# Kernel optimization log

Hardware: AMD Instinct MI355X
Metric: run time of the kernel (lower is better)

Reference implementation:

```python
import jax, jax.numpy as jnp
import numpy as np

B, S, H, NH = 8, 1024, 512, 8
HD = H // NH  # 64
ALPHA = 32.0


def setup_inputs() -> dict:
    key = jax.random.key(0)
    ks = jax.random.split(key, 8)
    hidden_states = jax.random.normal(ks[0], (B, S, H), dtype=jnp.float32)
    attention_mask = jnp.zeros((B, 1, 1, S), dtype=jnp.float32)
    rel_2d_pos = jax.random.normal(ks[1], (B, NH, S, S), dtype=jnp.float32)
    scale = 0.02
    Wq = jax.random.normal(ks[2], (H, H), dtype=jnp.float32) * scale
    Wk = jax.random.normal(ks[3], (H, H), dtype=jnp.float32) * scale
    Wv = jax.random.normal(ks[4], (H, H), dtype=jnp.float32) * scale
    bq = jnp.zeros((H,), dtype=jnp.float32)
    bk = jnp.zeros((H,), dtype=jnp.float32)
    bv = jnp.zeros((H,), dtype=jnp.float32)
    return {
        "hidden_states": hidden_states,
        "attention_mask": attention_mask,
        "rel_2d_pos": rel_2d_pos,
        "Wq": Wq, "bq": bq, "Wk": Wk, "bk": bk, "Wv": Wv, "bv": bv,
    }


def cogview_attention(scores, alpha=ALPHA):
    # scores / alpha -> amax -> softmax((s - max) * alpha); faithful to original
    scaled = scores / alpha
    max_value = jnp.max(scaled, axis=-1, keepdims=True)
    return jax.nn.softmax((scaled - max_value) * alpha, axis=-1)


def reference(hidden_states, attention_mask, rel_2d_pos, Wq, bq, Wk, bk, Wv, bv):
    b, s, _ = hidden_states.shape
    def split_heads(x):
        return x.reshape(b, s, NH, HD).transpose(0, 2, 1, 3)  # [B,NH,S,HD]
    q = split_heads(hidden_states @ Wq.T + bq)
    k = split_heads(hidden_states @ Wk.T + bk)
    v = split_heads(hidden_states @ Wv.T + bv)
    scale = 1.0 / jnp.sqrt(jnp.float32(HD))
    scores = jnp.einsum("bhqd,bhkd->bhqk", q * scale, k)
    scores = scores + rel_2d_pos  # spatial 2D relative bias
    scores = scores + attention_mask  # additive mask, broadcast [B,1,1,S]
    probs = cogview_attention(scores)
    ctx = jnp.einsum("bhqk,bhkd->bhqd", probs, v)
    ctx = ctx.transpose(0, 2, 1, 3).reshape(b, s, H)
    return ctx
```

## Files before the change

### kernel.cpp

```cpp
#include <hip/hip_runtime.h>

typedef _Float16 f16x8 __attribute__((ext_vector_type(8)));
typedef float    f32x4 __attribute__((ext_vector_type(4)));

#define MFMA16(a,b,c) __builtin_amdgcn_mfma_f32_16x16x32_f16((a),(b),(c),0,0,0)

constexpr int Bc  = 8;
constexpr int Sc  = 1024;
constexpr int Hc  = 512;
constexpr int NHc = 8;
constexpr int HDc = 64;

__global__ __launch_bounds__(256) void qkv_proj(
    const float* __restrict__ hs,
    const float* __restrict__ Wq, const float* __restrict__ bq,
    const float* __restrict__ Wk, const float* __restrict__ bk,
    const float* __restrict__ Wv, const float* __restrict__ bv,
    _Float16* __restrict__ qws, _Float16* __restrict__ kws,
    _Float16* __restrict__ vws)
{
    const int z  = blockIdx.z;
    const float* W   = (z == 0) ? Wq : (z == 1) ? Wk : Wv;
    const float* bia = (z == 0) ? bq : (z == 1) ? bk : bv;

    const int m0 = blockIdx.x * 64;
    const int n0 = blockIdx.y * 64;
    const int tid  = threadIdx.x;
    const int w    = tid >> 6;
    const int lane = tid & 63;
    const int l15  = lane & 15;
    const int quad = lane >> 4;

    __shared__ __align__(16) _Float16 As[64][40];
    __shared__ __align__(16) _Float16 Bs[64][40];

    f32x4 acc[4] = {};

    const int r = tid >> 2;
    const int c = (tid & 3) * 8;

    for (int kt = 0; kt < 16; ++kt) {
        const int k0 = kt * 32;
        const float4* ap = (const float4*)(hs + (size_t)(m0 + r) * 512 + k0 + c);
        const float4* bp = (const float4*)(W  + (size_t)(n0 + r) * 512 + k0 + c);
        float4 a0 = ap[0], a1 = ap[1];
        float4 b0 = bp[0], b1 = bp[1];
        __syncthreads();
        f16x8 av, bv8;
        av[0]=(_Float16)a0.x; av[1]=(_Float16)a0.y; av[2]=(_Float16)a0.z; av[3]=(_Float16)a0.w;
        av[4]=(_Float16)a1.x; av[5]=(_Float16)a1.y; av[6]=(_Float16)a1.z; av[7]=(_Float16)a1.w;
        bv8[0]=(_Float16)b0.x; bv8[1]=(_Float16)b0.y; bv8[2]=(_Float16)b0.z; bv8[3]=(_Float16)b0.w;
        bv8[4]=(_Float16)b1.x; bv8[5]=(_Float16)b1.y; bv8[6]=(_Float16)b1.z; bv8[7]=(_Float16)b1.w;
        *(f16x8*)&As[r][c] = av;
        *(f16x8*)&Bs[r][c] = bv8;
        __syncthreads();
        f16x8 af = *(const f16x8*)&As[w * 16 + l15][quad * 8];
#pragma unroll
        for (int nb = 0; nb < 4; ++nb) {
            f16x8 bf = *(const f16x8*)&Bs[nb * 16 + l15][quad * 8];
            acc[nb] = MFMA16(af, bf, acc[nb]);
        }
    }

#pragma unroll
    for (int nb = 0; nb < 4; ++nb) {
        const int n  = n0 + nb * 16 + l15;
        const float bvv = bia[n];
        const int h  = n >> 6;
        const int hd = n & 63;
#pragma unroll
        for (int rr = 0; rr < 4; ++rr) {
            const int m = m0 + w * 16 + quad * 4 + rr;
            const int b = m >> 10;
            const int s = m & 1023;
            const float val = acc[nb][rr] + bvv;
            if (z == 0)
                qws[(((size_t)(b * NHc + h)) * Sc + s) * HDc + hd] = (_Float16)val;
            else if (z == 1)
                kws[(((size_t)(b * NHc + h)) * Sc + s) * HDc + hd] = (_Float16)val;
            else
                vws[(((size_t)(b * NHc + h)) * HDc + hd) * Sc + s] = (_Float16)val;
        }
    }
}

__global__ __launch_bounds__(256) void attn(
    const _Float16* __restrict__ qws, const _Float16* __restrict__ kws,
    const _Float16* __restrict__ vws, const float* __restrict__ rel,
    const float* __restrict__ mask, float* __restrict__ out)
{
    const int qt = blockIdx.x;
    const int bh = blockIdx.y;
    const int b  = bh >> 3;
    const int h  = bh & 7;
    const int tid  = threadIdx.x;
    const int w    = tid >> 6;
    const int lane = tid & 63;
    const int l15  = lane & 15;
    const int quad = lane >> 4;
    const int q0w  = qt * 64 + w * 16;

    __shared__ __align__(16) _Float16 lds_p[4][16][72];

    const _Float16* qh = qws + (size_t)bh * Sc * HDc;
    const _Float16* kh = kws + (size_t)bh * Sc * HDc;
    const _Float16* vh = vws + (size_t)bh * HDc * Sc;
    const float* relh  = rel + (size_t)bh * Sc * Sc;
    const float* maskb = mask + (size_t)b * Sc;

    f16x8 qf0 = *(const f16x8*)(qh + (size_t)(q0w + l15) * HDc + quad * 8);
    f16x8 qf1 = *(const f16x8*)(qh + (size_t)(q0w + l15) * HDc + 32 + quad * 8);

    float m_run[4], l_run[4];
    f32x4 o[4] = {};
#pragma unroll
    for (int rj = 0; rj < 4; ++rj) { m_run[rj] = -1e30f; l_run[rj] = 0.f; }

    for (int kt = 0; kt < 16; ++kt) {
        const int kbase = kt * 64;

        f32x4 sc[4] = {};
#pragma unroll
        for (int nb = 0; nb < 4; ++nb) {
            const _Float16* kp = kh + (size_t)(kbase + nb * 16 + l15) * HDc + quad * 8;
            f16x8 kf0 = *(const f16x8*)kp;
            f16x8 kf1 = *(const f16x8*)(kp + 32);
            sc[nb] = MFMA16(qf0, kf0, sc[nb]);
            sc[nb] = MFMA16(qf1, kf1, sc[nb]);
        }

#pragma unroll
        for (int nb = 0; nb < 4; ++nb) {
            const int kcol = kbase + nb * 16 + l15;
            const float mk = maskb[kcol];
#pragma unroll
            for (int rj = 0; rj < 4; ++rj) {
                const int qrow = q0w + quad * 4 + rj;
                sc[nb][rj] = sc[nb][rj] * 0.125f + relh[(size_t)qrow * Sc + kcol] + mk;
            }
        }

#pragma unroll
        for (int rj = 0; rj < 4; ++rj) {
            float mx = fmaxf(fmaxf(sc[0][rj], sc[1][rj]), fmaxf(sc[2][rj], sc[3][rj]));
#pragma unroll
            for (int off = 1; off < 16; off <<= 1) mx = fmaxf(mx, __shfl_xor(mx, off));
            const float mnew  = fmaxf(m_run[rj], mx);
            const float alpha = __expf(m_run[rj] - mnew);
            float rs = 0.f;
#pragma unroll
            for (int nb = 0; nb < 4; ++nb) {
                const float p = __expf(sc[nb][rj] - mnew);
                sc[nb][rj] = p;
                rs += p;
            }
#pragma unroll
            for (int off = 1; off < 16; off <<= 1) rs += __shfl_xor(rs, off);
            m_run[rj] = mnew;
            l_run[rj] = l_run[rj] * alpha + rs;
            o[0][rj] *= alpha; o[1][rj] *= alpha; o[2][rj] *= alpha; o[3][rj] *= alpha;
        }

        __syncthreads();
#pragma unroll
        for (int nb = 0; nb < 4; ++nb)
#pragma unroll
            for (int rj = 0; rj < 4; ++rj)
                lds_p[w][quad * 4 + rj][nb * 16 + l15] = (_Float16)sc[nb][rj];
        __syncthreads();
        f16x8 ap0 = *(const f16x8*)&lds_p[w][l15][quad * 8];
        f16x8 ap1 = *(const f16x8*)&lds_p[w][l15][32 + quad * 8];

#pragma unroll
        for (int nb = 0; nb < 4; ++nb) {
            const _Float16* vp = vh + (size_t)(nb * 16 + l15) * Sc + kbase + quad * 8;
            f16x8 v0 = *(const f16x8*)vp;
            f16x8 v1 = *(const f16x8*)(vp + 32);
            o[nb] = MFMA16(ap0, v0, o[nb]);
            o[nb] = MFMA16(ap1, v1, o[nb]);
        }
    }

#pragma unroll
    for (int nb = 0; nb < 4; ++nb) {
#pragma unroll
        for (int rj = 0; rj < 4; ++rj) {
            const int qrow = q0w + quad * 4 + rj;
            out[((size_t)(b * Sc + qrow)) * Hc + h * HDc + nb * 16 + l15] =
                o[nb][rj] / l_run[rj];
        }
    }
}

extern "C" void kernel_launch(void* const* d_in, const int* in_sizes, int n_in,
                              void* d_out, int out_size, void* d_ws, size_t ws_size,
                              hipStream_t stream) {
    const float* hs   = (const float*)d_in[0];
    const float* mask = (const float*)d_in[1];
    const float* rel  = (const float*)d_in[2];
    const float* Wq   = (const float*)d_in[3];
    const float* bq   = (const float*)d_in[4];
    const float* Wk   = (const float*)d_in[5];
    const float* bk   = (const float*)d_in[6];
    const float* Wv   = (const float*)d_in[7];
    const float* bv   = (const float*)d_in[8];
    float* out = (float*)d_out;

    const size_t elems = (size_t)Bc * Sc * Hc;
    _Float16* qws = (_Float16*)d_ws;
    _Float16* kws = qws + elems;
    _Float16* vws = kws + elems;

    qkv_proj<<<dim3(128, 8, 3), 256, 0, stream>>>(hs, Wq, bq, Wk, bk, Wv, bv,
                                                  qws, kws, vws);
    attn<<<dim3(16, 64), 256, 0, stream>>>(qws, kws, vws, rel, mask, out);
}
```

Measured before the change: 510.5 us.

## Pre-convert inputs to fp16, use larger-tile QKV GEMM, prefetch rel bias

A separate kernel now converts hidden states and the three weight matrices to fp16. The QKV projection becomes one fused GEMM with 128x128 tiles and 16 accumulators per wave, loading tiles through global_load_lds. The attention kernel prefetches the next tile's rel_2d_pos values into registers, drops the block-wide barriers around the per-wave LDS probability tile, and multiplies by a reciprocal at the end. This trades an extra conversion pass and more registers for better GEMM reuse and latency hiding on the large fp32 bias stream. Removing the barriers relies on each wave using only its own LDS slice.

```diff
diff --git a/kernel.cpp b/kernel.cpp
--- a/kernel.cpp
+++ b/kernel.cpp
@@ -1,6 +1,7 @@
 #include <hip/hip_runtime.h>
 
 typedef _Float16 f16x8 __attribute__((ext_vector_type(8)));
+typedef _Float16 f16x4 __attribute__((ext_vector_type(4)));
 typedef float    f32x4 __attribute__((ext_vector_type(4)));
 
 #define MFMA16(a,b,c) __builtin_amdgcn_mfma_f32_16x16x32_f16((a),(b),(c),0,0,0)
@@ -11,75 +12,119 @@
 constexpr int NHc = 8;
 constexpr int HDc = 64;
 
-__global__ __launch_bounds__(256) void qkv_proj(
+__global__ __launch_bounds__(256) void cvt_f16(
     const float* __restrict__ hs,
-    const float* __restrict__ Wq, const float* __restrict__ bq,
-    const float* __restrict__ Wk, const float* __restrict__ bk,
-    const float* __restrict__ Wv, const float* __restrict__ bv,
+    const float* __restrict__ wq, const float* __restrict__ wk,
+    const float* __restrict__ wv,
+    _Float16* __restrict__ hs16, _Float16* __restrict__ w16)
+{
+    const size_t i4  = (size_t)blockIdx.x * 256 + threadIdx.x;
+    const size_t HS4 = (size_t)Bc * Sc * Hc / 4;
+    const size_t W4  = (size_t)Hc * Hc / 4;
+    float4 v;
+    _Float16* dst;
+    if (i4 < HS4) {
+        v = ((const float4*)hs)[i4];
+        dst = hs16 + i4 * 4;
+    } else {
+        const size_t j = i4 - HS4;
+        const int z = (int)(j / W4);
+        const size_t o = j - (size_t)z * W4;
+        const float* src = (z == 0) ? wq : (z == 1) ? wk : wv;
+        v = ((const float4*)src)[o];
+        dst = w16 + j * 4;
+    }
+    f16x4 h;
+    h[0] = (_Float16)v.x; h[1] = (_Float16)v.y;
+    h[2] = (_Float16)v.z; h[3] = (_Float16)v.w;
+    *(f16x4*)dst = h;
+}
+
+__global__ __launch_bounds__(256) void qkv_gemm(
+    const _Float16* __restrict__ A,
+    const _Float16* __restrict__ Bm,
+    const float* __restrict__ bq, const float* __restrict__ bk,
+    const float* __restrict__ bv,
     _Float16* __restrict__ qws, _Float16* __restrict__ kws,
     _Float16* __restrict__ vws)
 {
-    const int z  = blockIdx.z;
-    const float* W   = (z == 0) ? Wq : (z == 1) ? Wk : Wv;
-    const float* bia = (z == 0) ? bq : (z == 1) ? bk : bv;
-
-    const int m0 = blockIdx.x * 64;
-    const int n0 = blockIdx.y * 64;
+    __shared__ __align__(16) _Float16 As[128 * 64];
+    __shared__ __align__(16) _Float16 Bs[128 * 64];
+
+    const int m0 = blockIdx.x * 128;
+    const int n0 = blockIdx.y * 128;
     const int tid  = threadIdx.x;
+    const int lane = tid & 63;
     const int w    = tid >> 6;
-    const int lane = tid & 63;
     const int l15  = lane & 15;
     const int quad = lane >> 4;
-
-    __shared__ __align__(16) _Float16 As[64][40];
-    __shared__ __align__(16) _Float16 Bs[64][40];
-
-    f32x4 acc[4] = {};
-
-    const int r = tid >> 2;
-    const int c = (tid & 3) * 8;
-
-    for (int kt = 0; kt < 16; ++kt) {
-        const int k0 = kt * 32;
-        const float4* ap = (const float4*)(hs + (size_t)(m0 + r) * 512 + k0 + c);
-        const float4* bp = (const float4*)(W  + (size_t)(n0 + r) * 512 + k0 + c);
-        float4 a0 = ap[0], a1 = ap[1];
-        float4 b0 = bp[0], b1 = bp[1];
+    const int wm   = (w >> 1) * 64;
+    const int wn   = (w & 1) * 64;
+
+    f32x4 acc[4][4] = {};
+
+    const int srow = tid >> 3;
+    const int scol = (tid & 7) * 8;
+
+    for (int k0 = 0; k0 < 512; k0 += 64) {
         __syncthreads();
-        f16x8 av, bv8;
-        av[0]=(_Float16)a0.x; av[1]=(_Float16)a0.y; av[2]=(_Float16)a0.z; av[3]=(_Float16)a0.w;
-        av[4]=(_Float16)a1.x; av[5]=(_Float16)a1.y; av[6]=(_Float16)a1.z; av[7]=(_Float16)a1.w;
-        bv8[0]=(_Float16)b0.x; bv8[1]=(_Float16)b0.y; bv8[2]=(_Float16)b0.z; bv8[3]=(_Float16)b0.w;
-        bv8[4]=(_Float16)b1.x; bv8[5]=(_Float16)b1.y; bv8[6]=(_Float16)b1.z; bv8[7]=(_Float16)b1.w;
-        *(f16x8*)&As[r][c] = av;
-        *(f16x8*)&Bs[r][c] = bv8;
+#pragma unroll
+        for (int j = 0; j < 4; ++j) {
+            const _Float16* ga = A  + (size_t)(m0 + srow + 32 * j) * 512 + k0 + scol;
+            const _Float16* gb = Bm + (size_t)(n0 + srow + 32 * j) * 512 + k0 + scol;
+            __builtin_amdgcn_global_load_lds(
+                (const __attribute__((address_space(1))) void*)ga,
+                (__attribute__((address_space(3))) void*)(As + tid * 8 + j * 2048),
+                16, 0, 0);
+            __builtin_amdgcn_global_load_lds(
+                (const __attribute__((address_space(1))) void*)gb,
+                (__attribute__((address_space(3))) void*)(Bs + tid * 8 + j * 2048),
+                16, 0, 0);
+        }
         __syncthreads();
-        f16x8 af = *(const f16x8*)&As[w * 16 + l15][quad * 8];
-#pragma unroll
-        for (int nb = 0; nb < 4; ++nb) {
-            f16x8 bf = *(const f16x8*)&Bs[nb * 16 + l15][quad * 8];
-            acc[nb] = MFMA16(af, bf, acc[nb]);
-        }
-    }
-
+#pragma unroll
+        for (int ks = 0; ks < 2; ++ks) {
+            f16x8 af[4], bf[4];
+#pragma unroll
+            for (int i = 0; i < 4; ++i) {
+                af[i] = *(const f16x8*)&As[(wm + i * 16 + l15) * 64 + ks * 32 + quad * 8];
+                bf[i] = *(const f16x8*)&Bs[(wn + i * 16 + l15) * 64 + ks * 32 + quad * 8];
+            }
+#pragma unroll
+            for (int mb = 0; mb < 4; ++mb)
+#pragma unroll
+                for (int nb = 0; nb < 4; ++nb)
+                    acc[mb][nb] = MFMA16(af[mb], bf[nb], acc[mb][nb]);
+        }
+    }
+
+    const int zsel = n0 >> 9;
+    const float* bias = (zsel == 0) ? bq : (zsel == 1) ? bk : bv;
 #pragma unroll
     for (int nb = 0; nb < 4; ++nb) {
-        const int n  = n0 + nb * 16 + l15;
-        const float bvv = bia[n];
-        const int h  = n >> 6;
-        const int hd = n & 63;
-#pragma unroll
-        for (int rr = 0; rr < 4; ++rr) {
-            const int m = m0 + w * 16 + quad * 4 + rr;
+        const int n  = n0 + wn + nb * 16 + l15;
+        const int nn = n & 511;
+        const int h  = nn >> 6;
+        const int hd = nn & 63;
+        const float bvv = bias[nn];
+#pragma unroll
+        for (int mb = 0; mb < 4; ++mb) {
+            const int m = m0 + wm + mb * 16 + quad * 4;
             const int b = m >> 10;
             const int s = m & 1023;
-            const float val = acc[nb][rr] + bvv;
-            if (z == 0)
-                qws[(((size_t)(b * NHc + h)) * Sc + s) * HDc + hd] = (_Float16)val;
-            else if (z == 1)
-                kws[(((size_t)(b * NHc + h)) * Sc + s) * HDc + hd] = (_Float16)val;
-            else
-                vws[(((size_t)(b * NHc + h)) * HDc + hd) * Sc + s] = (_Float16)val;
+            if (zsel == 2) {
+                f16x4 t;
+#pragma unroll
+                for (int rr = 0; rr < 4; ++rr)
+                    t[rr] = (_Float16)(acc[mb][nb][rr] + bvv);
+                *(f16x4*)&vws[((size_t)(b * NHc + h) * HDc + hd) * Sc + s] = t;
+            } else {
+                _Float16* dst = (zsel == 0 ? qws : kws)
+                              + ((size_t)(b * NHc + h) * Sc + s) * HDc + hd;
+#pragma unroll
+                for (int rr = 0; rr < 4; ++rr)
+                    dst[(size_t)rr * HDc] = (_Float16)(acc[mb][nb][rr] + bvv);
+            }
         }
     }
 }
@@ -116,6 +161,15 @@
 #pragma unroll
     for (int rj = 0; rj < 4; ++rj) { m_run[rj] = -1e30f; l_run[rj] = 0.f; }
 
+    float rbuf[16];
+#pragma unroll
+    for (int nb = 0; nb < 4; ++nb)
+#pragma unroll
+        for (int rj = 0; rj < 4; ++rj)
+            rbuf[nb * 4 + rj] =
+                relh[(size_t)(q0w + quad * 4 + rj) * Sc + nb * 16 + l15];
+
+#pragma unroll
     for (int kt = 0; kt < 16; ++kt) {
         const int kbase = kt * 64;
 
@@ -129,15 +183,23 @@
             sc[nb] = MFMA16(qf1, kf1, sc[nb]);
         }
 
+        float rn[16];
+        if (kt < 15) {
+#pragma unroll
+            for (int nb = 0; nb < 4; ++nb)
+#pragma unroll
+                for (int rj = 0; rj < 4; ++rj)
+                    rn[nb * 4 + rj] =
+                        relh[(size_t)(q0w + quad * 4 + rj) * Sc
+                             + kbase + 64 + nb * 16 + l15];
+        }
+
 #pragma unroll
         for (int nb = 0; nb < 4; ++nb) {
-            const int kcol = kbase + nb * 16 + l15;
-            const float mk = maskb[kcol];
-#pragma unroll
-            for (int rj = 0; rj < 4; ++rj) {
-                const int qrow = q0w + quad * 4 + rj;
-                sc[nb][rj] = sc[nb][rj] * 0.125f + relh[(size_t)qrow * Sc + kcol] + mk;
-            }
+            const float mk = maskb[kbase + nb * 16 + l15];
+#pragma unroll
+            for (int rj = 0; rj < 4; ++rj)
+                sc[nb][rj] = sc[nb][rj] * 0.125f + rbuf[nb * 4 + rj] + mk;
         }
 
 #pragma unroll
@@ -161,13 +223,11 @@
             o[0][rj] *= alpha; o[1][rj] *= alpha; o[2][rj] *= alpha; o[3][rj] *= alpha;
         }
 
-        __syncthreads();
 #pragma unroll
         for (int nb = 0; nb < 4; ++nb)
 #pragma unroll
             for (int rj = 0; rj < 4; ++rj)
                 lds_p[w][quad * 4 + rj][nb * 16 + l15] = (_Float16)sc[nb][rj];
-        __syncthreads();
         f16x8 ap0 = *(const f16x8*)&lds_p[w][l15][quad * 8];
         f16x8 ap1 = *(const f16x8*)&lds_p[w][l15][32 + quad * 8];
 
@@ -179,16 +239,19 @@
             o[nb] = MFMA16(ap0, v0, o[nb]);
             o[nb] = MFMA16(ap1, v1, o[nb]);
         }
-    }
-
-#pragma unroll
-    for (int nb = 0; nb < 4; ++nb) {
-#pragma unroll
-        for (int rj = 0; rj < 4; ++rj) {
-            const int qrow = q0w + quad * 4 + rj;
+
+#pragma unroll
+        for (int i = 0; i < 16; ++i) rbuf[i] = rn[i];
+    }
+
+#pragma unroll
+    for (int rj = 0; rj < 4; ++rj) {
+        const float linv = 1.0f / l_run[rj];
+        const int qrow = q0w + quad * 4 + rj;
+#pragma unroll
+        for (int nb = 0; nb < 4; ++nb)
             out[((size_t)(b * Sc + qrow)) * Hc + h * HDc + nb * 16 + l15] =
-                o[nb][rj] / l_run[rj];
-        }
+                o[nb][rj] * linv;
     }
 }
 
@@ -207,11 +270,15 @@
     float* out = (float*)d_out;
 
     const size_t elems = (size_t)Bc * Sc * Hc;
-    _Float16* qws = (_Float16*)d_ws;
-    _Float16* kws = qws + elems;
-    _Float16* vws = kws + elems;
-
-    qkv_proj<<<dim3(128, 8, 3), 256, 0, stream>>>(hs, Wq, bq, Wk, bk, Wv, bv,
-                                                  qws, kws, vws);
+    _Float16* hs16 = (_Float16*)d_ws;
+    _Float16* w16  = hs16 + elems;
+    _Float16* qws  = w16 + (size_t)3 * Hc * Hc;
+    _Float16* kws  = qws + elems;
+    _Float16* vws  = kws + elems;
+
+    const int cvt_blocks = (int)(((size_t)Bc * Sc * Hc + 3 * Hc * Hc) / 4 / 256);
+    cvt_f16<<<cvt_blocks, 256, 0, stream>>>(hs, Wq, Wk, Wv, hs16, w16);
+    qkv_gemm<<<dim3(64, 12), 256, 0, stream>>>(hs16, w16, bq, bk, bv,
+                                               qws, kws, vws);
     attn<<<dim3(16, 64), 256, 0, stream>>>(qws, kws, vws, rel, mask, out);
 }
```

Result: slower. 641.0 us (+25.6%).
